# Kernel tuning notes

Hardware: AMD Instinct MI355X
Metric: run time of the kernel (lower is better)

Reference implementation:

```python
import jax, jax.numpy as jnp
import numpy as np

B, NQ, NC = 4, 512, 2048
DQ, DC, C = 1024, 768, 1024
H = 16
HD = C // H
L = 2
EPS = 1e-5


def _ln(x, g, b):
    m = jnp.mean(x, axis=-1, keepdims=True)
    v = jnp.mean((x - m) ** 2, axis=-1, keepdims=True)
    return (x - m) * jax.lax.rsqrt(v + EPS) * g + b


def setup_inputs() -> dict:
    key = jax.random.key(0)
    ks = iter(jax.random.split(key, 16))
    s = 0.02
    inp = {}
    inp['query'] = jax.random.normal(next(ks), (B, NQ, DQ), dtype=jnp.float32)
    inp['context'] = jax.random.normal(next(ks), (B, NC, DC), dtype=jnp.float32)
    mask = jax.random.randint(next(ks), (B, NC), 0, 2, dtype=jnp.int32)
    inp['context_mask'] = mask.at[:, 0].set(1)  # guarantee >=1 valid key per row
    inp['Wqp'] = jax.random.normal(next(ks), (DQ, C), dtype=jnp.float32) * s
    inp['bqp'] = jnp.zeros((C,), jnp.float32)
    inp['Wcp'] = jax.random.normal(next(ks), (DC, C), dtype=jnp.float32) * s
    inp['bcp'] = jnp.zeros((C,), jnp.float32)
    inp['Wq'] = jax.random.normal(next(ks), (L, C, C), dtype=jnp.float32) * s
    inp['bq'] = jnp.zeros((L, C), jnp.float32)
    inp['Wkv'] = jax.random.normal(next(ks), (L, C, 2 * C), dtype=jnp.float32) * s
    inp['bkv'] = jnp.zeros((L, 2 * C), jnp.float32)
    inp['Wo'] = jax.random.normal(next(ks), (L, C, C), dtype=jnp.float32) * s
    inp['bo'] = jnp.zeros((L, C), jnp.float32)
    inp['g1'] = jnp.ones((L, C), jnp.float32)
    inp['beta1'] = jnp.zeros((L, C), jnp.float32)
    inp['W1'] = jax.random.normal(next(ks), (L, C, 4 * C), dtype=jnp.float32) * s
    inp['bf1'] = jnp.zeros((L, 4 * C), jnp.float32)
    inp['W2'] = jax.random.normal(next(ks), (L, 4 * C, C), dtype=jnp.float32) * s
    inp['bf2'] = jnp.zeros((L, C), jnp.float32)
    inp['g2'] = jnp.ones((L, C), jnp.float32)
    inp['beta2'] = jnp.zeros((L, C), jnp.float32)
    inp['gf'] = jnp.ones((C,), jnp.float32)
    inp['betaf'] = jnp.zeros((C,), jnp.float32)
    return inp


def reference(query, context, context_mask, Wqp, bqp, Wcp, bcp, Wq, bq, Wkv, bkv,
              Wo, bo, g1, beta1, W1, bf1, W2, bf2, g2, beta2, gf, betaf):
    scale = HD ** -0.5
    q = query @ Wqp + bqp            # [B,NQ,C]
    c = context @ Wcp + bcp          # [B,NC,C]
    neg = (context_mask == 0)[:, None, None, :]  # [B,1,1,NC]
    for l in range(L):
        qn = _ln(q, g1[l], beta1[l])
        qh = (qn @ Wq[l] + bq[l]).reshape(B, NQ, H, HD).transpose(0, 2, 1, 3)
        kv = (c @ Wkv[l] + bkv[l]).reshape(B, NC, 2, H, HD).transpose(2, 0, 3, 1, 4)
        k, v = kv[0], kv[1]          # [B,H,NC,HD]
        attn = jnp.einsum('bhqd,bhkd->bhqk', qh, k) * scale
        attn = jnp.where(neg, -jnp.inf, attn)
        attn = jax.nn.softmax(attn, axis=-1)
        out = jnp.einsum('bhqk,bhkd->bhqd', attn, v)
        out = out.transpose(0, 2, 1, 3).reshape(B, NQ, C)
        q = q + (out @ Wo[l] + bo[l])
        h = _ln(q, g2[l], beta2[l])
        q = q + (jax.nn.gelu(h @ W1[l] + bf1[l], approximate=False) @ W2[l] + bf2[l])
    return _ln(q, gf, betaf)
```

## Files before the change

### kernel.cpp

```cpp
#include <hip/hip_runtime.h>
#include <hip/hip_bf16.h>
#include <math.h>

typedef __hip_bfloat16 bf16;
using short8 = __attribute__((ext_vector_type(8))) short;
using f32x4  = __attribute__((ext_vector_type(4))) float;

#define B_    4
#define NQ_   512
#define NC_   2048
#define DQ_   1024
#define DC_   768
#define C_    1024
#define H_    16
#define HD_   64
#define EPS_  1e-5f

__device__ __forceinline__ float ldin(const void* p, size_t i, int f32) {
    return f32 ? ((const float*)p)[i]
               : __bfloat162float(((const bf16*)p)[i]);
}
__device__ __forceinline__ unsigned bfb(float f) {
    return (unsigned)__builtin_bit_cast(unsigned short, __float2bfloat16(f));
}

typedef const __attribute__((address_space(1))) unsigned int ga_u32;
typedef __attribute__((address_space(3))) unsigned int ls_u32;
__device__ __forceinline__ void gl16(const void* g, void* l) {
    __builtin_amdgcn_global_load_lds((ga_u32*)g, (ls_u32*)l, 16, 0, 0);
}

__global__ __launch_bounds__(256)
void sniff_k(const void* __restrict__ q, int* __restrict__ flag)
{
    __shared__ int red[256];
    const unsigned* w = (const unsigned*)q;
    const int t = threadIdx.x;
    int cnt = 0;
    for (int i = t; i < 1024; i += 256) {
        unsigned e = (w[i] >> 7) & 0xFFu;
        cnt += (e >= 0x70u && e <= 0x82u) ? 1 : 0;
    }
    red[t] = cnt; __syncthreads();
    for (int s = 128; s > 0; s >>= 1) { if (t < s) red[t] += red[t + s]; __syncthreads(); }
    if (t == 0) flag[0] = (red[0] > 512) ? 0 : 1;
}

__global__ __launch_bounds__(256)
void cvt_k(const void* __restrict__ src, bf16* __restrict__ dst, int n8,
           const int* __restrict__ dtf)
{
    const int i = blockIdx.x * 256 + threadIdx.x;
    if (i >= n8) return;
    if (dtf[0]) {
        const float* s = (const float*)src + (size_t)i * 8;
        float4 a = *(const float4*)s, b = *(const float4*)(s + 4);
        uint4 o;
        o.x = bfb(a.x) | (bfb(a.y) << 16);
        o.y = bfb(a.z) | (bfb(a.w) << 16);
        o.z = bfb(b.x) | (bfb(b.y) << 16);
        o.w = bfb(b.z) | (bfb(b.w) << 16);
        *(uint4*)(dst + (size_t)i * 8) = o;
    } else {
        *(uint4*)(dst + (size_t)i * 8) = *(const uint4*)((const bf16*)src + (size_t)i * 8);
    }
}

struct KTr {
    const void* src[6];
    bf16*       dst[6];
    long long   off[6];
    int ld[6], K[6], N[6];
    int start[7];
    int njobs;
};

__global__ __launch_bounds__(256)
void tr_all(KTr J, const int* __restrict__ dtf)
{
    __shared__ short T[64 * 65];
    const int f32 = dtf[0];
    const int t = threadIdx.x;
    int bid = blockIdx.x, j = 0;
    while (j + 1 < J.njobs && bid >= J.start[j + 1]) ++j;
    const int tt = bid - J.start[j];
    const int nx = J.N[j] >> 6;
    const int n0 = (tt % nx) * 64, k0 = (tt / nx) * 64;
    const int ld = J.ld[j], K = J.K[j];
    {
        const int k = t >> 2, nq = (t & 3) * 16;
        size_t si = (size_t)J.off[j] + (size_t)(k0 + k) * ld + n0 + nq;
        short v[16];
        if (f32) {
            const float* s = (const float*)J.src[j] + si;
#pragma unroll
            for (int u = 0; u < 4; u++) {
                float4 f = *(const float4*)(s + u * 4);
                v[u*4+0] = (short)bfb(f.x); v[u*4+1] = (short)bfb(f.y);
                v[u*4+2] = (short)bfb(f.z); v[u*4+3] = (short)bfb(f.w);
            }
        } else {
            const bf16* s = (const bf16*)J.src[j] + si;
#pragma unroll
            for (int u = 0; u < 2; u++) {
                uint4 x = *(const uint4*)(s + u * 8);
                unsigned a[4] = {x.x, x.y, x.z, x.w};
#pragma unroll
                for (int m = 0; m < 4; m++) {
                    v[u*8 + m*2]     = (short)(a[m] & 0xffffu);
                    v[u*8 + m*2 + 1] = (short)(a[m] >> 16);
                }
            }
        }
#pragma unroll
        for (int jj = 0; jj < 16; jj++) T[k * 65 + nq + jj] = v[jj];
    }
    __syncthreads();
    {
        const int n = t >> 2, kq = (t & 3) * 16;
        unsigned pk[8];
#pragma unroll
        for (int u = 0; u < 8; u++) {
            unsigned lo = (unsigned short)T[(kq + u*2)     * 65 + n];
            unsigned hi = (unsigned short)T[(kq + u*2 + 1) * 65 + n];
            pk[u] = lo | (hi << 16);
        }
        bf16* d = J.dst[j] + (size_t)(n0 + n) * K + k0 + kq;
        *(uint4*)(d)     = make_uint4(pk[0], pk[1], pk[2], pk[3]);
        *(uint4*)(d + 8) = make_uint4(pk[4], pk[5], pk[6], pk[7]);
    }
}

template<int ACT, int ACC, int OUTF32, int BN>
__global__ __launch_bounds__(256)
void gemm_bf(const bf16* __restrict__ A, int lda,
             const bf16* __restrict__ Wt,
             const void* __restrict__ bias, size_t boff, float bscale,
             void* __restrict__ outp, int M, int N, int K,
             const int* __restrict__ dtf)
{
    __shared__ short As[2][128 * 32];
    __shared__ short Bs[2][BN * 32];
    constexpr int MI = (BN == 128) ? 4 : 2;
    const int t  = threadIdx.x;
    const int nwg = gridDim.x * gridDim.y;
    int flat = blockIdx.y * gridDim.x + blockIdx.x;
    flat = (flat & 7) * (nwg >> 3) + (flat >> 3);
    const int row0 = (flat / gridDim.x) * 128, col0 = (flat % gridDim.x) * BN;
    const int wv = t >> 6, l = t & 63;
    const int lm = l & 15, lq = l >> 4;
    const int lr = l >> 2, lc = l & 3;
    const int swc  = lc ^ ((lr >> 1) & 3);
    const int koff = (lq ^ ((lm >> 1) & 3)) << 3;
    const int wr = (BN == 128) ? (wv >> 1) * 64 : wv * 32;
    const int wc = (BN == 128) ? (wv & 1) * 64 : 0;

    const bf16* Ag0 = A + (size_t)(row0 + wv * 32 + lr) * lda + swc * 8;
    const bf16* Ag1 = Ag0 + (size_t)16 * lda;
    const bf16* Bg0 = Wt + (size_t)(col0 + ((BN == 128) ? wv * 32 : wv * 16) + lr) * K + swc * 8;
    const bf16* Bg1 = (BN == 128) ? (Bg0 + (size_t)16 * K) : Bg0;

    f32x4 acc[MI][4];
#pragma unroll
    for (int i = 0; i < MI; i++)
#pragma unroll
        for (int j = 0; j < 4; j++) { acc[i][j][0]=0.f; acc[i][j][1]=0.f; acc[i][j][2]=0.f; acc[i][j][3]=0.f; }

    auto stage = [&](int b, int k0) {
        gl16(Ag0 + k0, &As[b][(wv * 32) * 32]);
        gl16(Ag1 + k0, &As[b][(wv * 32 + 16) * 32]);
        if constexpr (BN == 128) {
            gl16(Bg0 + k0, &Bs[b][(wv * 32) * 32]);
            gl16(Bg1 + k0, &Bs[b][(wv * 32 + 16) * 32]);
        } else {
            gl16(Bg0 + k0, &Bs[b][(wv * 16) * 32]);
        }
    };

    const int nt = K >> 5;
    stage(0, 0);
    __syncthreads();
    int cur = 0;
    for (int tt = 0; tt < nt; ++tt) {
        if (tt + 1 < nt) stage(cur ^ 1, (tt + 1) * 32);
        short8 af[MI], bfr[4];
#pragma unroll
        for (int i = 0; i < MI; i++) af[i]  = *(const short8*)&As[cur][(wr + i*16 + lm) * 32 + koff];
#pragma unroll
        for (int j = 0; j < 4; j++)  bfr[j] = *(const short8*)&Bs[cur][(wc + j*16 + lm) * 32 + koff];
#pragma unroll
        for (int i = 0; i < MI; i++)
#pragma unroll
            for (int j = 0; j < 4; j++)
                acc[i][j] = __builtin_amdgcn_mfma_f32_16x16x32_bf16(af[i], bfr[j], acc[i][j], 0, 0, 0);
        __syncthreads();
        cur ^= 1;
    }

    const int fb = dtf[0];
#pragma unroll
    for (int i = 0; i < MI; i++) {
#pragma unroll
        for (int j = 0; j < 4; j++) {
            const int cgl = col0 + wc + j * 16 + lm;
            const float bsv = bscale * ldin(bias, boff + cgl, fb);
#pragma unroll
            for (int r = 0; r < 4; r++) {
                const int rgl = row0 + wr + i * 16 + lq * 4 + r;
                float v = acc[i][j][r] + bsv;
                if (ACT == 1) v = 0.5f * v * (1.0f + erff(v * 0.70710678118654752440f));
                size_t o = (size_t)rgl * N + cgl;
                if constexpr (ACC)          ((float*)outp)[o] += v;
                else if constexpr (OUTF32)  ((float*)outp)[o] = v;
                else                        ((bf16*)outp)[o] = __float2bfloat16(v);
            }
        }
    }
}

__global__ __launch_bounds__(256)
void gemm_kv(const bf16* __restrict__ A, int lda,
             const bf16* __restrict__ Wt,
             const void* __restrict__ bias, size_t boff,
             bf16* __restrict__ kb, bf16* __restrict__ vt,
             int M, int K, const int* __restrict__ dtf)
{
    __shared__ short smem[17408];
    const int t  = threadIdx.x;
    const int nwg = gridDim.x * gridDim.y;
    int flat = blockIdx.y * gridDim.x + blockIdx.x;
    flat = (flat & 7) * (nwg >> 3) + (flat >> 3);
    const int row0 = (flat / gridDim.x) * 128, col0 = (flat % gridDim.x) * 128;
    const int wv = t >> 6, l = t & 63;
    const int lm = l & 15, lq = l >> 4;
    const int lr = l >> 2, lc = l & 3;
    const int swc  = lc ^ ((lr >> 1) & 3);
    const int koff = (lq ^ ((lm >> 1) & 3)) << 3;
    const int wr = (wv >> 1) * 64, wc = (wv & 1) * 64;

    const bf16* Ag0 = A + (size_t)(row0 + wv * 32 + lr) * lda + swc * 8;
    const bf16* Ag1 = Ag0 + (size_t)16 * lda;
    const bf16* Bg0 = Wt + (size_t)(col0 + wv * 32 + lr) * K + swc * 8;
    const bf16* Bg1 = Bg0 + (size_t)16 * K;

    f32x4 acc[4][4];
#pragma unroll
    for (int i = 0; i < 4; i++)
#pragma unroll
        for (int j = 0; j < 4; j++) { acc[i][j][0]=0.f; acc[i][j][1]=0.f; acc[i][j][2]=0.f; acc[i][j][3]=0.f; }

    auto stage = [&](int b, int k0) {
        gl16(Ag0 + k0, &smem[b * 4096 + (wv * 32) * 32]);
        gl16(Ag1 + k0, &smem[b * 4096 + (wv * 32 + 16) * 32]);
        gl16(Bg0 + k0, &smem[8192 + b * 4096 + (wv * 32) * 32]);
        gl16(Bg1 + k0, &smem[8192 + b * 4096 + (wv * 32 + 16) * 32]);
    };

    const int nt = K >> 5;
    stage(0, 0);
    __syncthreads();
    int cur = 0;
    for (int tt = 0; tt < nt; ++tt) {
        if (tt + 1 < nt) stage(cur ^ 1, (tt + 1) * 32);
        short8 af[4], bfr[4];
#pragma unroll
        for (int i = 0; i < 4; i++) af[i]  = *(const short8*)&smem[cur * 4096 + (wr + i*16 + lm) * 32 + koff];
#pragma unroll
        for (int j = 0; j < 4; j++) bfr[j] = *(const short8*)&smem[8192 + cur * 4096 + (wc + j*16 + lm) * 32 + koff];
#pragma unroll
        for (int i = 0; i < 4; i++)
#pragma unroll
            for (int j = 0; j < 4; j++)
                acc[i][j] = __builtin_amdgcn_mfma_f32_16x16x32_bf16(af[i], bfr[j], acc[i][j], 0, 0, 0);
        __syncthreads();
        cur ^= 1;
    }

    const int fb = dtf[0];
    if (col0 < C_) {
#pragma unroll
        for (int i = 0; i < 4; i++)
#pragma unroll
            for (int j = 0; j < 4; j++) {
                const int cgl = col0 + wc + j * 16 + lm;
                const float bsv = ldin(bias, boff + cgl, fb);
#pragma unroll
                for (int r = 0; r < 4; r++) {
                    const int rgl = row0 + wr + i * 16 + lq * 4 + r;
                    kb[(size_t)rgl * C_ + cgl] = __float2bfloat16(acc[i][j][r] + bsv);
                }
            }
    } else {
#pragma unroll
        for (int i = 0; i < 4; i++)
#pragma unroll
            for (int j = 0; j < 4; j++) {
                const int cl = wc + j * 16 + lm;
                const float bsv = ldin(bias, boff + col0 + cl, fb);
                unsigned p0 = bfb(acc[i][j][0] + bsv) | (bfb(acc[i][j][1] + bsv) << 16);
                unsigned p1 = bfb(acc[i][j][2] + bsv) | (bfb(acc[i][j][3] + bsv) << 16);
                *(uint2*)&smem[cl * 136 + wr + i * 16 + lq * 4] = make_uint2(p0, p1);
            }
        __syncthreads();
        const int dr = t >> 1, half = (t & 1) * 64;
        const int b = row0 >> 11, key0 = row0 & (NC_ - 1);
        bf16* dst = vt + (size_t)b * C_ * NC_ + (size_t)(col0 - C_ + dr) * NC_ + key0 + half;
#pragma unroll
        for (int u = 0; u < 8; u++)
            *(uint4*)(dst + u * 8) = *(const uint4*)&smem[dr * 136 + half + u * 8];
    }
}

template<int OFINAL>
__global__ __launch_bounds__(256)
void ln_k(const float* __restrict__ x, const void* __restrict__ g,
          const void* __restrict__ b, size_t gboff, void* __restrict__ out,
          const int* __restrict__ dtf)
{
    __shared__ float red[256];
    const int f32 = dtf[0];
    const int row = blockIdx.x;
    const int t = threadIdx.x;
    const float* xr = x + (size_t)row * C_;
    float v[4];
#pragma unroll
    for (int i = 0; i < 4; i++) v[i] = xr[t + 256 * i];
    float s = v[0] + v[1] + v[2] + v[3];
    red[t] = s; __syncthreads();
    for (int st = 128; st > 0; st >>= 1) { if (t < st) red[t] += red[t + st]; __syncthreads(); }
    float mean = red[0] * (1.0f / C_);
    __syncthreads();
    float s2 = 0.f;
#pragma unroll
    for (int i = 0; i < 4; i++) { float d = v[i] - mean; s2 += d * d; }
    red[t] = s2; __syncthreads();
    for (int st = 128; st > 0; st >>= 1) { if (t < st) red[t] += red[t + st]; __syncthreads(); }
    float rstd = rsqrtf(red[0] * (1.0f / C_) + EPS_);
#pragma unroll
    for (int i = 0; i < 4; i++) {
        int cc = t + 256 * i;
        float r = (v[i] - mean) * rstd * ldin(g, gboff + cc, f32) + ldin(b, gboff + cc, f32);
        size_t o = (size_t)row * C_ + cc;
        if constexpr (OFINAL) {
            if (f32) ((float*)out)[o] = r; else ((bf16*)out)[o] = __float2bfloat16(r);
        } else {
            ((bf16*)out)[o] = __float2bfloat16(r);
        }
    }
}

__global__ __launch_bounds__(256)
void attn_mfma(const bf16* __restrict__ qh, const bf16* __restrict__ kb,
               const bf16* __restrict__ vt, const int* __restrict__ mask,
               bf16* __restrict__ out)
{
    __shared__ short Ks[64 * 72];
    __shared__ short Vs[64 * 72];
    __shared__ short Ps[4][16 * 72];

    const int id = blockIdx.x;
    const int xcd = id & 7, kk = id >> 3;
    const int p = xcd + ((kk >> 3) << 3);
    const int bb = p >> 4, h = p & 15, q0 = (kk & 7) * 64;

    const bf16* qhb = qh + (size_t)bb * NQ_ * C_;
    const bf16* kbb = kb + (size_t)bb * NC_ * C_;
    const bf16* vtb = vt + (size_t)bb * C_ * NC_ + (size_t)h * HD_ * NC_;
    const int*  mb  = mask + bb * NC_;
    bf16* ob = out + (size_t)bb * NQ_ * C_;

    const int t  = threadIdx.x;
    const int w  = t >> 6, l = t & 63;
    const int lm = l & 15, lq = l >> 4;
    short* Pw = Ps[w];

    short8 qf[2];
    {
        const bf16* qp = qhb + (size_t)(q0 + w * 16 + lm) * C_ + h * HD_ + lq * 8;
        qf[0] = *(const short8*)(qp);
        qf[1] = *(const short8*)(qp + 32);
    }

    f32x4 o[4];
#pragma unroll
    for (int jd = 0; jd < 4; jd++) { o[jd][0]=0.f; o[jd][1]=0.f; o[jd][2]=0.f; o[jd][3]=0.f; }
    float m_run[4], l_run[4];
#pragma unroll
    for (int r = 0; r < 4; r++) { m_run[r] = -1e30f; l_run[r] = 0.f; }

    const int kr = t >> 2, c16 = (t & 3) * 16;
    const bf16* kg = kbb + (size_t)kr * C_ + h * HD_ + c16;
    const bf16* vg = vtb + (size_t)kr * NC_ + c16;

    uint4 ka, kb2, va, vb2;
    int mk[4];
    {
        ka  = *(const uint4*)(kg);
        kb2 = *(const uint4*)(kg + 8);
        va  = *(const uint4*)(vg);
        vb2 = *(const uint4*)(vg + 8);
#pragma unroll
        for (int jt = 0; jt < 4; jt++) mk[jt] = mb[jt * 16 + lm];
    }

    for (int k0 = 0; k0 < NC_; k0 += 64) {
        __syncthreads();
        *(uint4*)&Ks[kr * 72 + c16]     = ka;
        *(uint4*)&Ks[kr * 72 + c16 + 8] = kb2;
        *(uint4*)&Vs[kr * 72 + c16]     = va;
        *(uint4*)&Vs[kr * 72 + c16 + 8] = vb2;
        int mc[4];
#pragma unroll
        for (int jt = 0; jt < 4; jt++) mc[jt] = mk[jt];
        __syncthreads();

        if (k0 + 64 < NC_) {
            ka  = *(const uint4*)(kg + (size_t)(k0 + 64) * C_);
            kb2 = *(const uint4*)(kg + (size_t)(k0 + 64) * C_ + 8);
            va  = *(const uint4*)(vg + k0 + 64);
            vb2 = *(const uint4*)(vg + k0 + 64 + 8);
#pragma unroll
            for (int jt = 0; jt < 4; jt++) mk[jt] = mb[k0 + 64 + jt * 16 + lm];
        }

        f32x4 s[4];
#pragma unroll
        for (int jt = 0; jt < 4; jt++) { s[jt][0]=0.f; s[jt][1]=0.f; s[jt][2]=0.f; s[jt][3]=0.f; }
        __builtin_amdgcn_s_setprio(1);
#pragma unroll
        for (int dc = 0; dc < 2; dc++) {
#pragma unroll
            for (int jt = 0; jt < 4; jt++) {
                short8 kf = *(const short8*)&Ks[(jt * 16 + lm) * 72 + dc * 32 + lq * 8];
                s[jt] = __builtin_amdgcn_mfma_f32_16x16x32_bf16(qf[dc], kf, s[jt], 0, 0, 0);
            }
        }
        __builtin_amdgcn_s_setprio(0);
#pragma unroll
        for (int jt = 0; jt < 4; jt++) {
#pragma unroll
            for (int r = 0; r < 4; r++)
                s[jt][r] = mc[jt] ? s[jt][r] * 0.125f : -1e30f;
        }

#pragma unroll
        for (int r = 0; r < 4; r++) {
            float mt = fmaxf(fmaxf(s[0][r], s[1][r]), fmaxf(s[2][r], s[3][r]));
#pragma unroll
            for (int sh = 1; sh < 16; sh <<= 1) mt = fmaxf(mt, __shfl_xor(mt, sh, 64));
            const float nm = fmaxf(m_run[r], mt);
            const float al = __expf(m_run[r] - nm);
            float p0 = __expf(s[0][r] - nm);
            float p1 = __expf(s[1][r] - nm);
            float p2 = __expf(s[2][r] - nm);
            float p3 = __expf(s[3][r] - nm);
            short* pr = &Pw[(lq * 4 + r) * 72 + lm];
            pr[0]  = (short)bfb(p0);
            pr[16] = (short)bfb(p1);
            pr[32] = (short)bfb(p2);
            pr[48] = (short)bfb(p3);
            float rs = p0 + p1 + p2 + p3;
#pragma unroll
            for (int sh = 1; sh < 16; sh <<= 1) rs += __shfl_xor(rs, sh, 64);
            l_run[r] = l_run[r] * al + rs;
            m_run[r] = nm;
#pragma unroll
            for (int jd = 0; jd < 4; jd++) o[jd][r] *= al;
        }

        short8 pa0 = *(const short8*)&Pw[lm * 72 + lq * 8];
        short8 pa1 = *(const short8*)&Pw[lm * 72 + 32 + lq * 8];
        __builtin_amdgcn_s_setprio(1);
#pragma unroll
        for (int jd = 0; jd < 4; jd++) {
            short8 v0 = *(const short8*)&Vs[(jd * 16 + lm) * 72 + lq * 8];
            short8 v1 = *(const short8*)&Vs[(jd * 16 + lm) * 72 + 32 + lq * 8];
            o[jd] = __builtin_amdgcn_mfma_f32_16x16x32_bf16(pa0, v0, o[jd], 0, 0, 0);
            o[jd] = __builtin_amdgcn_mfma_f32_16x16x32_bf16(pa1, v1, o[jd], 0, 0, 0);
        }
        __builtin_amdgcn_s_setprio(0);
    }

#pragma unroll
    for (int r = 0; r < 4; r++) {
        const float inv = 1.0f / l_run[r];
        bf16* dst = ob + (size_t)(q0 + w * 16 + lq * 4 + r) * C_ + h * HD_ + lm;
#pragma unroll
        for (int jd = 0; jd < 4; jd++) dst[jd * 16] = __float2bfloat16(o[jd][r] * inv);
    }
}

static void add_job(KTr& J, const void* src, long long off, int ld,
                    bf16* dst, int K, int N)
{
    const int j = J.njobs++;
    J.src[j] = src; J.off[j] = off; J.ld[j] = ld;
    J.dst[j] = dst; J.K[j] = K; J.N[j] = N;
    J.start[j + 1] = J.start[j] + (N / 64) * (K / 64);
}

extern "C" void kernel_launch(void* const* d_in, const int* in_sizes, int n_in,
                              void* d_out, int out_size, void* d_ws, size_t ws_size,
                              hipStream_t stream)
{
    const void* query   = d_in[0];
    const void* context = d_in[1];
    const int*  mask    = (const int*)d_in[2];
    const void* Wqp = d_in[3];  const void* bqp  = d_in[4];
    const void* Wcp = d_in[5];  const void* bcp  = d_in[6];
    const void* Wq  = d_in[7];  const void* bq   = d_in[8];
    const void* Wkv = d_in[9];  const void* bkv  = d_in[10];
    const void* Wo  = d_in[11]; const void* bo   = d_in[12];
    const void* g1  = d_in[13]; const void* be1  = d_in[14];
    const void* W1  = d_in[15]; const void* bf1  = d_in[16];
    const void* W2  = d_in[17]; const void* bf2  = d_in[18];
    const void* g2  = d_in[19]; const void* be2  = d_in[20];
    const void* gf  = d_in[21]; const void* bef  = d_in[22];

    char* w = (char*)d_ws;
    const bool mega = ws_size >= (((size_t)88 << 20) + 64);

    float* q    = (float*)(w);
    bf16*  xn   = (bf16*) (w + ( 8u << 20));
    bf16*  qh   = (bf16*) (w + (12u << 20));
    bf16*  ff1h = (bf16*) (w + (12u << 20));
    bf16*  cbf  = (bf16*) (w + (12u << 20));
    bf16*  qbf  = (bf16*) (w + (24u << 20));
    bf16*  kb   = (bf16*) (w + (16u << 20));
    bf16*  vt   = (bf16*) (w + (32u << 20));
    bf16*  cb   = (bf16*) (w + (48u << 20));
    bf16*  Wt   = (bf16*) (w + (64u << 20));
    int*   dtf  = (int*)  (w + (mega ? (88u << 20) : (68u << 20)));

    const int MQ = B_ * NQ_;
    dim3 blk(256);
    const size_t M1 = 1u << 20;

    sniff_k<<<1, blk, 0, stream>>>(query, dtf);

    cvt_k<<<dim3((MQ * DQ_) / 8 / 256), blk, 0, stream>>>(query, qbf, (MQ * DQ_) / 8, dtf);
    cvt_k<<<dim3((B_ * NC_ * DC_) / 8 / 256), blk, 0, stream>>>(context, cbf, (B_ * NC_ * DC_) / 8, dtf);

    bf16 *WqpT, *WcpT;
    if (mega) {
        KTr J{}; J.njobs = 0; J.start[0] = 0;
        WqpT = Wt; WcpT = Wt + M1;
        add_job(J, Wqp, 0, C_, WqpT, DQ_, C_);
        add_job(J, Wcp, 0, C_, WcpT, DC_, C_);
        tr_all<<<dim3(J.start[J.njobs]), blk, 0, stream>>>(J, dtf);
    } else {
        WqpT = WcpT = Wt;
        KTr J{}; J.njobs = 0; J.start[0] = 0;
        add_job(J, Wqp, 0, C_, Wt, DQ_, C_);
        tr_all<<<dim3(J.start[J.njobs]), blk, 0, stream>>>(J, dtf);
    }
    gemm_bf<0,0,1,64><<<dim3(C_/64, MQ/128), blk, 0, stream>>>(
        qbf, DQ_, WqpT, bqp, 0, 1.f, q, MQ, C_, DQ_, dtf);
    if (!mega) {
        KTr J{}; J.njobs = 0; J.start[0] = 0;
        add_job(J, Wcp, 0, C_, Wt, DC_, C_);
        tr_all<<<dim3(J.start[J.njobs]), blk, 0, stream>>>(J, dtf);
    }
    gemm_bf<0,0,0,128><<<dim3(C_/128, (B_*NC_)/128), blk, 0, stream>>>(
        cbf, DC_, WcpT, bcp, 0, 1.f, cb, B_*NC_, C_, DC_, dtf);

    for (int l = 0; l < 2; l++) {
        const size_t oC  = (size_t)l * C_;
        const size_t oCC = (size_t)l * C_ * C_;
        const size_t o2C = (size_t)l * 2 * C_;
        const size_t oK2 = (size_t)l * C_ * 2 * C_;
        const size_t o4C = (size_t)l * 4 * C_;
        const size_t oK4 = (size_t)l * C_ * 4 * C_;

        bf16 *WqT, *WkvT, *WoT, *W1T, *W2T;
        if (mega) {
            WqT = Wt; WkvT = Wt + M1; WoT = Wt + 3*M1; W1T = Wt + 4*M1; W2T = Wt + 8*M1;
            KTr J{}; J.njobs = 0; J.start[0] = 0;
            add_job(J, Wq,  (long long)oCC, C_,   WqT,  C_,   C_);
            add_job(J, Wkv, (long long)oK2, 2*C_, WkvT, C_,   2*C_);
            add_job(J, Wo,  (long long)oCC, C_,   WoT,  C_,   C_);
            add_job(J, W1,  (long long)oK4, 4*C_, W1T,  C_,   4*C_);
            add_job(J, W2,  (long long)oK4, C_,   W2T,  4*C_, C_);
            tr_all<<<dim3(J.start[J.njobs]), blk, 0, stream>>>(J, dtf);
        } else {
            WqT = WkvT = WoT = W1T = W2T = Wt;
        }

        ln_k<0><<<MQ, blk, 0, stream>>>(q, g1, be1, oC, xn, dtf);
        if (!mega) {
            KTr J{}; J.njobs = 0; J.start[0] = 0;
            add_job(J, Wq, (long long)oCC, C_, Wt, C_, C_);
            tr_all<<<dim3(J.start[J.njobs]), blk, 0, stream>>>(J, dtf);
        }
        gemm_bf<0,0,0,64><<<dim3(C_/64, MQ/128), blk, 0, stream>>>(
            xn, C_, WqT, bq, oC, 1.f, qh, MQ, C_, C_, dtf);

        if (!mega) {
            KTr J{}; J.njobs = 0; J.start[0] = 0;
            add_job(J, Wkv, (long long)oK2, 2*C_, Wt, C_, 2*C_);
            tr_all<<<dim3(J.start[J.njobs]), blk, 0, stream>>>(J, dtf);
        }
        gemm_kv<<<dim3((2*C_)/128, (B_*NC_)/128), blk, 0, stream>>>(
            cb, C_, WkvT, bkv, o2C, kb, vt, B_*NC_, C_, dtf);

        attn_mfma<<<dim3(512), blk, 0, stream>>>(qh, kb, vt, mask, qh);

        if (!mega) {
            KTr J{}; J.njobs = 0; J.start[0] = 0;
            add_job(J, Wo, (long long)oCC, C_, Wt, C_, C_);
            tr_all<<<dim3(J.start[J.njobs]), blk, 0, stream>>>(J, dtf);
        }
        gemm_bf<0,1,1,64><<<dim3(C_/64, MQ/128), blk, 0, stream>>>(
            qh, C_, WoT, bo, oC, 1.f, q, MQ, C_, C_, dtf);

        ln_k<0><<<MQ, blk, 0, stream>>>(q, g2, be2, oC, xn, dtf);
        if (mega) {
            gemm_bf<1,0,0,128><<<dim3((4*C_)/128, MQ/128), blk, 0, stream>>>(
                xn, C_, W1T, bf1, o4C, 1.f, ff1h, MQ, 4*C_, C_, dtf);
            gemm_bf<0,1,1,64><<<dim3(C_/64, MQ/128), blk, 0, stream>>>(
                ff1h, 4*C_, W2T, bf2, oC, 1.f, q, MQ, C_, 4*C_, dtf);
        } else {
            for (int hf = 0; hf < 2; hf++) {
                const long long w1off = (long long)oK4 + (long long)hf * 2048;
                const long long w2off = (long long)oK4 + (long long)hf * 2048 * C_;
                {
                    KTr J{}; J.njobs = 0; J.start[0] = 0;
                    add_job(J, W1, w1off, 4*C_, Wt, C_, 2048);
                    tr_all<<<dim3(J.start[J.njobs]), blk, 0, stream>>>(J, dtf);
                }
                gemm_bf<1,0,0,128><<<dim3(2048/128, MQ/128), blk, 0, stream>>>(
                    xn, C_, Wt, bf1, o4C + hf * 2048, 1.f, ff1h, MQ, 2048, C_, dtf);
                {
                    KTr J{}; J.njobs = 0; J.start[0] = 0;
                    add_job(J, W2, w2off, C_, Wt, 2048, C_);
                    tr_all<<<dim3(J.start[J.njobs]), blk, 0, stream>>>(J, dtf);
                }
                gemm_bf<0,1,1,64><<<dim3(C_/64, MQ/128), blk, 0, stream>>>(
                    ff1h, 2048, Wt, bf2, oC, (hf == 0) ? 1.f : 0.f, q, MQ, C_, 2048, dtf);
            }
        }
    }

    ln_k<1><<<MQ, blk, 0, stream>>>(q, gf, bef, 0, d_out, dtf);
}
```

Measured before the change: 800.2 us.

## Split attention over key range with merge kernel and widen key tile to 128

The attention kernel now processes 128-key tiles per iteration instead of 64, doubling LDS tiles and the per-iteration MFMA work. When the workspace is large enough it also splits the key dimension in two (flash-decoding style), launching 1024 blocks that write fp32 partial outputs, maxes and sums, then a separate merge kernel combines them into bf16. This targets low occupancy from only 512 blocks and per-tile sync overhead, at the cost of extra global traffic for the partials and an additional launch.

```diff
diff --git a/kernel.cpp b/kernel.cpp
--- a/kernel.cpp
+++ b/kernel.cpp
@@ -349,24 +349,32 @@
     }
 }
 
+template<int NSPLIT>
 __global__ __launch_bounds__(256)
 void attn_mfma(const bf16* __restrict__ qh, const bf16* __restrict__ kb,
                const bf16* __restrict__ vt, const int* __restrict__ mask,
-               bf16* __restrict__ out)
-{
-    __shared__ short Ks[64 * 72];
-    __shared__ short Vs[64 * 72];
-    __shared__ short Ps[4][16 * 72];
+               bf16* __restrict__ out,
+               float* __restrict__ po, float* __restrict__ pm,
+               float* __restrict__ pl)
+{
+    __shared__ short Ks[128 * 72];
+    __shared__ short Vs[64 * 136];
+    __shared__ short Ps[4][16 * 136];
 
     const int id = blockIdx.x;
     const int xcd = id & 7, kk = id >> 3;
     const int p = xcd + ((kk >> 3) << 3);
-    const int bb = p >> 4, h = p & 15, q0 = (kk & 7) * 64;
+    int bb, h, sp;
+    if constexpr (NSPLIT == 2) { bb = p >> 5; h = (p >> 1) & 15; sp = p & 1; }
+    else                       { bb = p >> 4; h = p & 15;        sp = 0;     }
+    const int q0 = (kk & 7) * 64;
+    const int kbase = sp * (NC_ / NSPLIT);
+    const int klen  = NC_ / NSPLIT;
 
     const bf16* qhb = qh + (size_t)bb * NQ_ * C_;
     const bf16* kbb = kb + (size_t)bb * NC_ * C_;
     const bf16* vtb = vt + (size_t)bb * C_ * NC_ + (size_t)h * HD_ * NC_;
-    const int*  mb  = mask + bb * NC_;
+    const int*  mb  = mask + bb * NC_ + kbase;
     bf16* ob = out + (size_t)bb * NQ_ * C_;
 
     const int t  = threadIdx.x;
@@ -388,56 +396,72 @@
 #pragma unroll
     for (int r = 0; r < 4; r++) { m_run[r] = -1e30f; l_run[r] = 0.f; }
 
-    const int kr = t >> 2, c16 = (t & 3) * 16;
-    const bf16* kg = kbb + (size_t)kr * C_ + h * HD_ + c16;
-    const bf16* vg = vtb + (size_t)kr * NC_ + c16;
-
-    uint4 ka, kb2, va, vb2;
-    int mk[4];
+    const int kr4 = t >> 2;
+    const int c16 = (t & 3) * 16;
+    const int c32 = (t & 3) * 32;
+    const bf16* kg = kbb + (size_t)(kbase + kr4) * C_ + h * HD_ + c16;
+    const bf16* vg = vtb + (size_t)kr4 * NC_ + kbase + c32;
+
+    uint4 k00, k01, k10, k11, v0, v1, v2, v3;
+    int mk[8];
     {
-        ka  = *(const uint4*)(kg);
-        kb2 = *(const uint4*)(kg + 8);
-        va  = *(const uint4*)(vg);
-        vb2 = *(const uint4*)(vg + 8);
-#pragma unroll
-        for (int jt = 0; jt < 4; jt++) mk[jt] = mb[jt * 16 + lm];
-    }
-
-    for (int k0 = 0; k0 < NC_; k0 += 64) {
+        k00 = *(const uint4*)(kg);
+        k01 = *(const uint4*)(kg + 8);
+        k10 = *(const uint4*)(kg + (size_t)64 * C_);
+        k11 = *(const uint4*)(kg + (size_t)64 * C_ + 8);
+        v0  = *(const uint4*)(vg);
+        v1  = *(const uint4*)(vg + 8);
+        v2  = *(const uint4*)(vg + 16);
+        v3  = *(const uint4*)(vg + 24);
+#pragma unroll
+        for (int jt = 0; jt < 8; jt++) mk[jt] = mb[jt * 16 + lm];
+    }
+
+    for (int k0 = 0; k0 < klen; k0 += 128) {
         __syncthreads();
-        *(uint4*)&Ks[kr * 72 + c16]     = ka;
-        *(uint4*)&Ks[kr * 72 + c16 + 8] = kb2;
-        *(uint4*)&Vs[kr * 72 + c16]     = va;
-        *(uint4*)&Vs[kr * 72 + c16 + 8] = vb2;
-        int mc[4];
-#pragma unroll
-        for (int jt = 0; jt < 4; jt++) mc[jt] = mk[jt];
+        *(uint4*)&Ks[kr4 * 72 + c16]            = k00;
+        *(uint4*)&Ks[kr4 * 72 + c16 + 8]        = k01;
+        *(uint4*)&Ks[(kr4 + 64) * 72 + c16]     = k10;
+        *(uint4*)&Ks[(kr4 + 64) * 72 + c16 + 8] = k11;
+        *(uint4*)&Vs[kr4 * 136 + c32]      = v0;
+        *(uint4*)&Vs[kr4 * 136 + c32 + 8]  = v1;
+        *(uint4*)&Vs[kr4 * 136 + c32 + 16] = v2;
+        *(uint4*)&Vs[kr4 * 136 + c32 + 24] = v3;
+        int mc[8];
+#pragma unroll
+        for (int jt = 0; jt < 8; jt++) mc[jt] = mk[jt];
         __syncthreads();
 
-        if (k0 + 64 < NC_) {
-            ka  = *(const uint4*)(kg + (size_t)(k0 + 64) * C_);
-            kb2 = *(const uint4*)(kg + (size_t)(k0 + 64) * C_ + 8);
-            va  = *(const uint4*)(vg + k0 + 64);
-            vb2 = *(const uint4*)(vg + k0 + 64 + 8);
-#pragma unroll
-            for (int jt = 0; jt < 4; jt++) mk[jt] = mb[k0 + 64 + jt * 16 + lm];
-        }
-
-        f32x4 s[4];
-#pragma unroll
-        for (int jt = 0; jt < 4; jt++) { s[jt][0]=0.f; s[jt][1]=0.f; s[jt][2]=0.f; s[jt][3]=0.f; }
+        if (k0 + 128 < klen) {
+            const bf16* kp = kg + (size_t)(k0 + 128) * C_;
+            k00 = *(const uint4*)(kp);
+            k01 = *(const uint4*)(kp + 8);
+            k10 = *(const uint4*)(kp + (size_t)64 * C_);
+            k11 = *(const uint4*)(kp + (size_t)64 * C_ + 8);
+            const bf16* vp = vg + k0 + 128;
+            v0 = *(const uint4*)(vp);
+            v1 = *(const uint4*)(vp + 8);
+            v2 = *(const uint4*)(vp + 16);
+            v3 = *(const uint4*)(vp + 24);
+#pragma unroll
+            for (int jt = 0; jt < 8; jt++) mk[jt] = mb[k0 + 128 + jt * 16 + lm];
+        }
+
+        f32x4 s[8];
+#pragma unroll
+        for (int jt = 0; jt < 8; jt++) { s[jt][0]=0.f; s[jt][1]=0.f; s[jt][2]=0.f; s[jt][3]=0.f; }
         __builtin_amdgcn_s_setprio(1);
 #pragma unroll
         for (int dc = 0; dc < 2; dc++) {
 #pragma unroll
-            for (int jt = 0; jt < 4; jt++) {
+            for (int jt = 0; jt < 8; jt++) {
                 short8 kf = *(const short8*)&Ks[(jt * 16 + lm) * 72 + dc * 32 + lq * 8];
                 s[jt] = __builtin_amdgcn_mfma_f32_16x16x32_bf16(qf[dc], kf, s[jt], 0, 0, 0);
             }
         }
         __builtin_amdgcn_s_setprio(0);
 #pragma unroll
-        for (int jt = 0; jt < 4; jt++) {
+        for (int jt = 0; jt < 8; jt++) {
 #pragma unroll
             for (int r = 0; r < 4; r++)
                 s[jt][r] = mc[jt] ? s[jt][r] * 0.125f : -1e30f;
@@ -445,21 +469,20 @@
 
 #pragma unroll
         for (int r = 0; r < 4; r++) {
-            float mt = fmaxf(fmaxf(s[0][r], s[1][r]), fmaxf(s[2][r], s[3][r]));
+            float mt = fmaxf(fmaxf(fmaxf(s[0][r], s[1][r]), fmaxf(s[2][r], s[3][r])),
+                             fmaxf(fmaxf(s[4][r], s[5][r]), fmaxf(s[6][r], s[7][r])));
 #pragma unroll
             for (int sh = 1; sh < 16; sh <<= 1) mt = fmaxf(mt, __shfl_xor(mt, sh, 64));
             const float nm = fmaxf(m_run[r], mt);
             const float al = __expf(m_run[r] - nm);
-            float p0 = __expf(s[0][r] - nm);
-            float p1 = __expf(s[1][r] - nm);
-            float p2 = __expf(s[2][r] - nm);
-            float p3 = __expf(s[3][r] - nm);
-            short* pr = &Pw[(lq * 4 + r) * 72 + lm];
-            pr[0]  = (short)bfb(p0);
-            pr[16] = (short)bfb(p1);
-            pr[32] = (short)bfb(p2);
-            pr[48] = (short)bfb(p3);
-            float rs = p0 + p1 + p2 + p3;
+            float rs = 0.f;
+            short* pr = &Pw[(lq * 4 + r) * 136 + lm];
+#pragma unroll
+            for (int jt = 0; jt < 8; jt++) {
+                float pv = __expf(s[jt][r] - nm);
+                pr[jt * 16] = (short)bfb(pv);
+                rs += pv;
+            }
 #pragma unroll
             for (int sh = 1; sh < 16; sh <<= 1) rs += __shfl_xor(rs, sh, 64);
             l_run[r] = l_run[r] * al + rs;
@@ -468,26 +491,62 @@
             for (int jd = 0; jd < 4; jd++) o[jd][r] *= al;
         }
 
-        short8 pa0 = *(const short8*)&Pw[lm * 72 + lq * 8];
-        short8 pa1 = *(const short8*)&Pw[lm * 72 + 32 + lq * 8];
+        short8 pa[4];
+#pragma unroll
+        for (int c = 0; c < 4; c++) pa[c] = *(const short8*)&Pw[lm * 136 + c * 32 + lq * 8];
         __builtin_amdgcn_s_setprio(1);
 #pragma unroll
         for (int jd = 0; jd < 4; jd++) {
-            short8 v0 = *(const short8*)&Vs[(jd * 16 + lm) * 72 + lq * 8];
-            short8 v1 = *(const short8*)&Vs[(jd * 16 + lm) * 72 + 32 + lq * 8];
-            o[jd] = __builtin_amdgcn_mfma_f32_16x16x32_bf16(pa0, v0, o[jd], 0, 0, 0);
-            o[jd] = __builtin_amdgcn_mfma_f32_16x16x32_bf16(pa1, v1, o[jd], 0, 0, 0);
+#pragma unroll
+            for (int c = 0; c < 4; c++) {
+                short8 vf = *(const short8*)&Vs[(jd * 16 + lm) * 136 + c * 32 + lq * 8];
+                o[jd] = __builtin_amdgcn_mfma_f32_16x16x32_bf16(pa[c], vf, o[jd], 0, 0, 0);
+            }
         }
         __builtin_amdgcn_s_setprio(0);
     }
 
-#pragma unroll
-    for (int r = 0; r < 4; r++) {
-        const float inv = 1.0f / l_run[r];
-        bf16* dst = ob + (size_t)(q0 + w * 16 + lq * 4 + r) * C_ + h * HD_ + lm;
-#pragma unroll
-        for (int jd = 0; jd < 4; jd++) dst[jd * 16] = __float2bfloat16(o[jd][r] * inv);
-    }
+    if constexpr (NSPLIT == 2) {
+        const int pidx = ((bb * 16 + h) * 2 + sp);
+#pragma unroll
+        for (int r = 0; r < 4; r++) {
+            const int row = q0 + w * 16 + lq * 4 + r;
+            float* prow = po + ((size_t)pidx * 512 + row) * 64;
+#pragma unroll
+            for (int jd = 0; jd < 4; jd++) prow[jd * 16 + lm] = o[jd][r];
+            if (lm == 0) {
+                pm[pidx * 512 + row] = m_run[r];
+                pl[pidx * 512 + row] = l_run[r];
+            }
+        }
+    } else {
+#pragma unroll
+        for (int r = 0; r < 4; r++) {
+            const float inv = 1.0f / l_run[r];
+            bf16* dst = ob + (size_t)(q0 + w * 16 + lq * 4 + r) * C_ + h * HD_ + lm;
+#pragma unroll
+            for (int jd = 0; jd < 4; jd++) dst[jd * 16] = __float2bfloat16(o[jd][r] * inv);
+        }
+    }
+}
+
+__global__ __launch_bounds__(256)
+void attn_merge(const float* __restrict__ po, const float* __restrict__ pm,
+                const float* __restrict__ pl, bf16* __restrict__ qh)
+{
+    const int t = threadIdx.x;
+    const int row = blockIdx.x * 4 + (t >> 6);
+    const int d = t & 63;
+    const int bh = row >> 9, qr = row & 511;
+    const int i0 = (bh * 2) * 512 + qr, i1 = i0 + 512;
+    const float m0 = pm[i0], m1 = pm[i1];
+    const float l0 = pl[i0], l1 = pl[i1];
+    const float nm = fmaxf(m0, m1);
+    const float e0 = __expf(m0 - nm), e1 = __expf(m1 - nm);
+    const float L = l0 * e0 + l1 * e1;
+    const float v = (po[(size_t)i0 * 64 + d] * e0 + po[(size_t)i1 * 64 + d] * e1) / L;
+    const int bb = bh >> 4, h = bh & 15;
+    qh[((size_t)bb * NQ_ + qr) * C_ + h * HD_ + d] = __float2bfloat16(v);
 }
 
 static void add_job(KTr& J, const void* src, long long off, int ld,
@@ -518,7 +577,8 @@
     const void* gf  = d_in[21]; const void* bef  = d_in[22];
 
     char* w = (char*)d_ws;
-    const bool mega = ws_size >= (((size_t)88 << 20) + 64);
+    const bool mega  = ws_size >= (((size_t)88 << 20) + 64);
+    const bool split = ws_size >= (((size_t)110 << 20) + 64);
 
     float* q    = (float*)(w);
     bf16*  xn   = (bf16*) (w + ( 8u << 20));
@@ -531,6 +591,9 @@
     bf16*  cb   = (bf16*) (w + (48u << 20));
     bf16*  Wt   = (bf16*) (w + (64u << 20));
     int*   dtf  = (int*)  (w + (mega ? (88u << 20) : (68u << 20)));
+    float* po   = (float*)(w + (90u << 20));
+    float* pm   = (float*)(w + (107u << 20));
+    float* pl   = (float*)(w + (107u << 20) + (256u << 10));
 
     const int MQ = B_ * NQ_;
     dim3 blk(256);
@@ -603,7 +666,12 @@
         gemm_kv<<<dim3((2*C_)/128, (B_*NC_)/128), blk, 0, stream>>>(
             cb, C_, WkvT, bkv, o2C, kb, vt, B_*NC_, C_, dtf);
 
-        attn_mfma<<<dim3(512), blk, 0, stream>>>(qh, kb, vt, mask, qh);
+        if (split) {
+            attn_mfma<2><<<dim3(1024), blk, 0, stream>>>(qh, kb, vt, mask, qh, po, pm, pl);
+            attn_merge<<<dim3(8192), blk, 0, stream>>>(po, pm, pl, qh);
+        } else {
+            attn_mfma<1><<<dim3(512), blk, 0, stream>>>(qh, kb, vt, mask, qh, po, pm, pl);
+        }
 
         if (!mega) {
             KTr J{}; J.njobs = 0; J.start[0] = 0;
```

Result: no change. 788.6 us (-1.5%).
